# Performance work log

Measured on AMD Instinct MI355X. Metric: run time of the kernel, lower is better.

Reference implementation:

```python
import jax, jax.numpy as jnp
import numpy as np
import math

B, S, DIM = 2, 2048, 2048
NH = 16
HD = DIM // NH  # 128
RANK = 32


def setup_inputs() -> dict:
    key = jax.random.key(0)
    ks = jax.random.split(key, 10)
    x = jax.random.normal(ks[0], (B, S, DIM), dtype=jnp.float32)
    # causal additive mask (use -1e9 instead of -inf for grad-safety)
    mask = jnp.where(jnp.tril(jnp.ones((S, S), dtype=bool)), 0.0, -1e9).astype(jnp.float32)[None, None]
    # rotary frequencies, as in llama: theta = 10000^{-2i/d}
    inv_freq = 1.0 / (10000.0 ** (jnp.arange(0, HD, 2, dtype=jnp.float32) / HD))  # [HD/2]
    t = jnp.arange(S, dtype=jnp.float32)
    freqs = jnp.outer(t, inv_freq)  # [S, HD/2]
    freqs_cos = jnp.cos(freqs)
    freqs_sin = jnp.sin(freqs)
    scale = 0.02
    wq = jax.random.normal(ks[1], (DIM, DIM), dtype=jnp.float32) * scale
    wk = jax.random.normal(ks[2], (DIM, DIM), dtype=jnp.float32) * scale
    wv = jax.random.normal(ks[3], (DIM, DIM), dtype=jnp.float32) * scale
    wo = jax.random.normal(ks[4], (DIM, DIM), dtype=jnp.float32) * scale
    wa_q = jax.random.normal(ks[5], (RANK, DIM), dtype=jnp.float32) * 0.02
    wa_k = jax.random.normal(ks[6], (RANK, DIM), dtype=jnp.float32) * 0.02
    return {"x": x, "mask": mask, "freqs_cos": freqs_cos, "freqs_sin": freqs_sin,
            "wq": wq, "wk": wk, "wv": wv, "wo": wo, "wa_q": wa_q, "wa_k": wa_k}


def _apply_rope(t, cos, sin):
    # t: [B, S, H, HD]; cos/sin: [S, HD/2]
    tr = t.reshape(*t.shape[:-1], HD // 2, 2)
    tre, tim = tr[..., 0], tr[..., 1]
    c = cos[None, :, None, :]
    s = sin[None, :, None, :]
    out_re = tre * c - tim * s
    out_im = tre * s + tim * c
    return jnp.stack([out_re, out_im], axis=-1).reshape(t.shape)


def reference(x, mask, freqs_cos, freqs_sin, wq, wk, wv, wo, wa_q, wa_k):
    bsz, seqlen, dim = x.shape
    xq = (x @ wq.T).reshape(bsz, seqlen, NH, HD)
    xk = (x @ wk.T).reshape(bsz, seqlen, NH, HD)
    xv = (x @ wv.T).reshape(bsz, seqlen, NH, HD)
    # low-rank adaptive gate (computed on detached x in the original)
    xd = jax.lax.stop_gradient(x)
    xq_h = xd @ wa_q.T  # [B, S, 32]
    xk_h = xd @ wa_k.T  # [B, S, 32]
    adaptive_mask = jnp.einsum('bqr,bkr->bqk', xq_h, xk_h)  # [B, S, S]

    xq = _apply_rope(xq, freqs_cos, freqs_sin)
    xk = _apply_rope(xk, freqs_cos, freqs_sin)

    q = xq.transpose(0, 2, 1, 3)  # [B, H, S, HD]
    k = xk.transpose(0, 2, 1, 3)
    v = xv.transpose(0, 2, 1, 3)

    scores = jnp.einsum('bhqd,bhkd->bhqk', q, k) / math.sqrt(HD)
    scores = scores + mask
    scores = jax.nn.softmax(scores.astype(jnp.float32), axis=-1).astype(q.dtype)
    scores = scores * jax.nn.sigmoid(adaptive_mask)[:, None]  # gate, broadcast over heads
    out = jnp.einsum('bhqk,bhkd->bhqd', scores, v)
    out = out.transpose(0, 2, 1, 3).reshape(bsz, seqlen, -1)
    return out @ wo.T
```

## Files before the change

### kernel.cpp

```cpp
#include <hip/hip_runtime.h>

typedef __attribute__((ext_vector_type(8))) short short8v;
typedef __attribute__((ext_vector_type(4))) short short4v;
typedef __attribute__((ext_vector_type(4))) float floatx4;

#define S_    2048
#define DIM_  2048
#define NW_   6400
#define VOFF_ 4352

#define ASG(p) ((__attribute__((address_space(1))) void*)(p))
#define ASL(p) ((__attribute__((address_space(3))) void*)(p))

__device__ __forceinline__ short f2bf(float f){
  union { float f; unsigned u; } c; c.f = f;
  unsigned u = c.u;
  unsigned r = (u + 0x7fffu + ((u >> 16) & 1u)) >> 16;
  return (short)r;
}
__device__ __forceinline__ float bf2f(short s){
  union { unsigned u; float f; } c; c.u = ((unsigned)(unsigned short)s) << 16;
  return c.f;
}

__global__ __launch_bounds__(256) void cvt_k(const float* __restrict__ in,
                                             short* __restrict__ out, int n){
  int i = blockIdx.x*256 + threadIdx.x;
  int idx = i*4;
  if (idx >= n) return;
  floatx4 v = *(const floatx4*)(in + idx);
  short4v o;
  o[0]=f2bf(v[0]); o[1]=f2bf(v[1]); o[2]=f2bf(v[2]); o[3]=f2bf(v[3]);
  *(short4v*)(out + idx) = o;
}

__global__ __launch_bounds__(256)
void cvt_w(const float* wq, const float* waq, const float* wak,
           const float* wk, const float* wv, const float* wo,
           short* Wcat, short* wob){
  const float* src; short* dst; int n;
  switch (blockIdx.y){
    case 0: src=wq;  dst=Wcat;                 n=4194304; break;
    case 1: src=waq; dst=Wcat+(size_t)2048*2048; n=65536; break;
    case 2: src=wak; dst=Wcat+(size_t)2080*2048; n=65536; break;
    case 3: src=wk;  dst=Wcat+(size_t)2112*2048; n=4194304; break;
    case 4: src=wv;  dst=Wcat+(size_t)4352*2048; n=4194304; break;
    case 5: src=wo;  dst=wob;                  n=4194304; break;
    default: {
      int idx = (blockIdx.x*256 + threadIdx.x)*4;
      if (idx < 393216){
        short4v z = {0,0,0,0};
        *(short4v*)(Wcat + (size_t)4160*2048 + idx) = z;
      }
      return;
    }
  }
  int idx = (blockIdx.x*256 + threadIdx.x)*4;
  if (idx >= n) return;
  floatx4 v = *(const floatx4*)(src + idx);
  short4v o;
  o[0]=f2bf(v[0]); o[1]=f2bf(v[1]); o[2]=f2bf(v[2]); o[3]=f2bf(v[3]);
  *(short4v*)(dst + idx) = o;
}

__global__ __launch_bounds__(512,2)
void gemm_qkv(const short* __restrict__ A, const short* __restrict__ B,
              short* __restrict__ Cout, short* __restrict__ Vt){
  __shared__ short SH[65536];
  const int K = 2048;
  int tid = threadIdx.x;
  int wave = tid>>6, lane = tid&63, quad = lane>>4, l16 = lane&15;
  int wm_i = wave>>2, wn_i = wave&3;

  int bid = blockIdx.x;
  int swz = (bid&7)*50 + (bid>>3);
  int m0 = (swz & 15)*256;
  int n0 = (swz >> 4)*256;

  int srow = tid>>2;
  int sseg = (tid&3) ^ ((srow ^ (srow>>2)) & 3);
  const short* aS = A + (size_t)(m0 + srow)*K + sseg*8;
  const short* bS = B + (size_t)(n0 + srow)*K + sseg*8;
  int sdst = wave*512;

  int sx   = (l16 ^ (l16>>2)) & 3;
  int aoff = (wm_i*128 + l16)*32 + (quad^sx)*8;
  int boff = (wn_i*64  + l16)*32 + (quad^sx)*8;

  floatx4 acc[8][4] = {};

#define QSTAGE(src, chunk) do{ \
    __builtin_amdgcn_global_load_lds(ASG(src), ASL(&SH[(chunk)+sdst]), 16, 0, 0); \
    __builtin_amdgcn_global_load_lds(ASG((src) + (size_t)128*2048), ASL(&SH[(chunk)+sdst+4096]), 16, 0, 0); \
  }while(0)
#define QBAR  asm volatile("s_barrier" ::: "memory")
#define QW4   asm volatile("s_waitcnt vmcnt(4)" ::: "memory")

  QSTAGE(aS,            0);
  QSTAGE(bS,        32768);
  QSTAGE(aS+32,      8192);
  QSTAGE(bS+32, 32768+8192);
  QW4; QBAR;

  for (int t=0; t<32; ++t){
    int buf = t&1, nb = buf^1;
    int k0n = ((t+1)&31)*64;
    int A0 = buf*16384,        A1 = A0+8192;
    int B0 = 32768+buf*16384,  B1 = B0+8192;
    int nA0 = nb*16384,        nA1 = nA0+8192;
    int nB0 = 32768+nb*16384,  nB1 = nB0+8192;
    short8v af[8], bf[2];

    #pragma unroll
    for (int mf=0; mf<8; ++mf) af[mf] = *(short8v*)&SH[A0 + mf*512 + aoff];
    bf[0] = *(short8v*)&SH[B0 +   0 + boff];
    bf[1] = *(short8v*)&SH[B0 + 512 + boff];
    QSTAGE(aS + k0n, nA0);
    QBAR;
    __builtin_amdgcn_s_setprio(1);
    #pragma unroll
    for (int mf=0; mf<8; ++mf){
      acc[mf][0] = __builtin_amdgcn_mfma_f32_16x16x32_bf16(af[mf], bf[0], acc[mf][0], 0,0,0);
      acc[mf][1] = __builtin_amdgcn_mfma_f32_16x16x32_bf16(af[mf], bf[1], acc[mf][1], 0,0,0);
    }
    __builtin_amdgcn_s_setprio(0);
    QBAR;

    bf[0] = *(short8v*)&SH[B0 + 1024 + boff];
    bf[1] = *(short8v*)&SH[B0 + 1536 + boff];
    QSTAGE(bS + k0n, nB0);
    QBAR;
    __builtin_amdgcn_s_setprio(1);
    #pragma unroll
    for (int mf=0; mf<8; ++mf){
      acc[mf][2] = __builtin_amdgcn_mfma_f32_16x16x32_bf16(af[mf], bf[0], acc[mf][2], 0,0,0);
      acc[mf][3] = __builtin_amdgcn_mfma_f32_16x16x32_bf16(af[mf], bf[1], acc[mf][3], 0,0,0);
    }
    __builtin_amdgcn_s_setprio(0);
    QW4;
    QBAR;

    #pragma unroll
    for (int mf=0; mf<8; ++mf) af[mf] = *(short8v*)&SH[A1 + mf*512 + aoff];
    bf[0] = *(short8v*)&SH[B1 +   0 + boff];
    bf[1] = *(short8v*)&SH[B1 + 512 + boff];
    QSTAGE(aS + k0n + 32, nA1);
    QBAR;
    __builtin_amdgcn_s_setprio(1);
    #pragma unroll
    for (int mf=0; mf<8; ++mf){
      acc[mf][0] = __builtin_amdgcn_mfma_f32_16x16x32_bf16(af[mf], bf[0], acc[mf][0], 0,0,0);
      acc[mf][1] = __builtin_amdgcn_mfma_f32_16x16x32_bf16(af[mf], bf[1], acc[mf][1], 0,0,0);
    }
    __builtin_amdgcn_s_setprio(0);
    QBAR;

    bf[0] = *(short8v*)&SH[B1 + 1024 + boff];
    bf[1] = *(short8v*)&SH[B1 + 1536 + boff];
    QSTAGE(bS + k0n + 32, nB1);
    QBAR;
    __builtin_amdgcn_s_setprio(1);
    #pragma unroll
    for (int mf=0; mf<8; ++mf){
      acc[mf][2] = __builtin_amdgcn_mfma_f32_16x16x32_bf16(af[mf], bf[0], acc[mf][2], 0,0,0);
      acc[mf][3] = __builtin_amdgcn_mfma_f32_16x16x32_bf16(af[mf], bf[1], acc[mf][3], 0,0,0);
    }
    __builtin_amdgcn_s_setprio(0);
    QW4;
    QBAR;
  }

  __syncthreads();

  if (n0 < VOFF_){
    #pragma unroll
    for (int mf=0; mf<8; ++mf)
      #pragma unroll
      for (int r=0; r<4; ++r){
        size_t gm = (size_t)(m0 + wm_i*128 + mf*16 + quad*4 + r);
        #pragma unroll
        for (int nf=0; nf<4; ++nf)
          Cout[gm*NW_ + n0 + wn_i*64 + nf*16 + l16] = f2bf(acc[mf][nf][r]);
      }
  } else {
    short* T = SH;
    #pragma unroll
    for (int mf=0; mf<8; ++mf){
      int mb = wm_i*128 + mf*16 + quad*4;
      int mc = mb>>3, mi = mb&7;
      #pragma unroll
      for (int nf=0; nf<4; ++nf){
        int n = wn_i*64 + nf*16 + l16;
        short4v p;
        p[0]=f2bf(acc[mf][nf][0]); p[1]=f2bf(acc[mf][nf][1]);
        p[2]=f2bf(acc[mf][nf][2]); p[3]=f2bf(acc[mf][nf][3]);
        *(short4v*)&T[n*256 + ((mc ^ (n&31))*8) + mi] = p;
      }
    }
    __syncthreads();
    int f = tid>>1, half = tid&1;
    size_t vbase = (size_t)(n0 - VOFF_ + f)*4096 + m0;
    #pragma unroll
    for (int c=0; c<16; ++c){
      int cc = half*16 + c;
      short8v v = *(short8v*)&T[f*256 + ((cc ^ (f&31))*8)];
      *(short8v*)&Vt[vbase + cc*8] = v;
    }
  }
#undef QSTAGE
#undef QBAR
#undef QW4
}

__global__ __launch_bounds__(256,4)
void gemm_nt_f32(const short* __restrict__ A, const short* __restrict__ B,
                 float* __restrict__ Cout, int M, int N, int K){
  __shared__ short As[128][64];
  __shared__ short Bs[128][64];
  int tid = threadIdx.x;
  int wave = tid>>6, lane = tid&63, quad = lane>>4, l16 = lane&15;
  int l7 = l16&7;
  int m0 = blockIdx.x*128, n0 = blockIdx.y*128;
  int wm = (wave>>1)*64, wn = (wave&1)*64;
  floatx4 acc[4][4] = {};

  int lr = lane>>3;
  int sw = (lane&7) ^ lr;
  const short* Abase = A + (size_t)(m0 + wave*32 + lr)*K + sw*8;
  const short* Bbase = B + (size_t)(n0 + wave*32 + lr)*K + sw*8;

  for (int k0 = 0; k0 < K; k0 += 64){
    __syncthreads();
    #pragma unroll
    for (int i=0;i<4;i++){
      __builtin_amdgcn_global_load_lds(ASG(Abase + (size_t)(i*8)*K + k0),
                                       ASL(&As[wave*32 + i*8][0]), 16, 0, 0);
      __builtin_amdgcn_global_load_lds(ASG(Bbase + (size_t)(i*8)*K + k0),
                                       ASL(&Bs[wave*32 + i*8][0]), 16, 0, 0);
    }
    __syncthreads();
    #pragma unroll
    for (int ks=0; ks<2; ks++){
      short8v af[4], bf[4];
      #pragma unroll
      for (int i=0;i<4;i++) af[i] = *(short8v*)&As[wm + i*16 + l16][((ks*4+quad)^l7)*8];
      #pragma unroll
      for (int j=0;j<4;j++) bf[j] = *(short8v*)&Bs[wn + j*16 + l16][((ks*4+quad)^l7)*8];
      #pragma unroll
      for (int i=0;i<4;i++)
        #pragma unroll
        for (int j=0;j<4;j++)
          acc[i][j] = __builtin_amdgcn_mfma_f32_16x16x32_bf16(af[i], bf[j], acc[i][j], 0,0,0);
    }
  }
  #pragma unroll
  for (int i=0;i<4;i++)
    #pragma unroll
    for (int r=0;r<4;r++){
      int gm = m0 + wm + i*16 + quad*4 + r;
      #pragma unroll
      for (int j=0;j<4;j++){
        int gn = n0 + wn + j*16 + l16;
        Cout[(size_t)gm*N + gn] = acc[i][j][r];
      }
    }
}

__global__ __launch_bounds__(256) void rope_k(short* __restrict__ X,
                                              const float* __restrict__ fcos,
                                              const float* __restrict__ fsin){
  int i = blockIdx.x*256 + threadIdx.x;
  int row = i >> 10;
  int p = i & 1023;
  int s = row & (S_-1);
  int pp = p & 63;
  float c = fcos[s*64+pp], sn = fsin[s*64+pp];
  size_t a = (size_t)row*NW_ + 2112 + p*2;
  int v = *(int*)(X + a);
  float re = bf2f((short)(v & 0xffff)), im = bf2f((short)(v >> 16));
  float orr = re*c - im*sn, oi = re*sn + im*c;
  *(int*)(X + a) = ((int)(unsigned short)f2bf(oi) << 16) | (unsigned short)f2bf(orr);
}

__global__ __launch_bounds__(256)
void gate_k(const short* __restrict__ X, short* __restrict__ G){
  int kt = blockIdx.x, qt = blockIdx.y, b = blockIdx.z;
  if (kt > qt) return;
  int tid = threadIdx.x, wave = tid>>6, lane = tid&63, quad = lane>>4, l16 = lane&15;
  const float NL2E = -1.44269504f;

  short8v qh = *(const short8v*)&X[(size_t)(b*2048 + qt*64 + wave*16 + l16)*NW_ + 2048 + quad*8];
  floatx4 am[4];
  #pragma unroll
  for (int j=0;j<4;j++){
    short8v kh = *(const short8v*)&X[(size_t)(b*2048 + kt*64 + j*16 + l16)*NW_ + 2080 + quad*8];
    floatx4 z = {0.f,0.f,0.f,0.f};
    am[j] = __builtin_amdgcn_mfma_f32_16x16x32_bf16(qh, kh, z, 0,0,0);
  }
  short* Gd = G + (((size_t)(b*32 + kt)*2048) + qt*64 + wave*16 + quad*4)*64 + l16*4;
  #pragma unroll
  for (int r=0;r<4;r++){
    short4v sv;
    #pragma unroll
    for (int j=0;j<4;j++){
      float g = __builtin_amdgcn_rcpf(1.f + __builtin_amdgcn_exp2f(am[j][r]*NL2E));
      sv[j] = f2bf(g);
    }
    *(short4v*)(Gd + (size_t)r*64) = sv;
  }
}

__global__ __launch_bounds__(256,2)
void flash_k(const short* __restrict__ Qc, const short* __restrict__ Vt,
             const short* __restrict__ G, const float* __restrict__ fcos,
             const float* __restrict__ fsin, short* __restrict__ O){
  int h = blockIdx.x, pi = blockIdx.y, b = blockIdx.z;
  int tid = threadIdx.x, wave = tid>>6, lane = tid&63, quad = lane>>4, l16 = lane&15;
  int l7 = l16&7;

  __shared__ short Ks [64][128];
  __shared__ short Vts[128][64];
  __shared__ short Ps [4][16][72];

  const float CS = 1.44269504f * 0.08838834764831845f;

  for (int ph = 0; ph < 2; ph++){
    int qt = ph ? pi : 31 - pi;
    int srow = qt*64 + wave*16 + l16;
    size_t qrow = (size_t)(b*2048 + srow);
    short8v qf[4];
    #pragma unroll
    for (int ks=0;ks<4;ks++)
      qf[ks] = *(const short8v*)&Qc[qrow*NW_ + h*128 + ks*32 + quad*8];
    #pragma unroll
    for (int ks=0;ks<4;ks++)
      #pragma unroll
      for (int jj=0;jj<4;jj++){
        float re = bf2f(qf[ks][2*jj]), im = bf2f(qf[ks][2*jj+1]);
        int p = ks*16 + quad*4 + jj;
        float c = fcos[srow*64 + p], sn = fsin[srow*64 + p];
        qf[ks][2*jj]   = f2bf(re*c - im*sn);
        qf[ks][2*jj+1] = f2bf(re*sn + im*c);
      }

    floatx4 oacc[8] = {};
    float lp[4] = {0.f,0.f,0.f,0.f};

    for (int kt=0; kt<=qt; kt++){
      int k0 = kt*64;
      __syncthreads();
      {
        const short* Ksrc = Qc + ((size_t)(b*2048 + k0 + wave*16))*NW_ + 2112 + h*128;
        int r4 = lane>>4, c16 = lane&15;
        #pragma unroll
        for (int j=0;j<4;j++)
          __builtin_amdgcn_global_load_lds(
            ASG(Ksrc + (size_t)(j*4 + r4)*NW_ + ((c16 ^ r4 ^ ((j&1)*4))*8)),
            ASL(&Ks[wave*16 + j*4][0]), 16, 0, 0);
        const short* Vsrc = Vt + ((size_t)(h*128 + wave*32 + (lane>>3)))*4096 + b*2048 + k0
                            + (((lane&7) ^ (lane>>3))*8);
        #pragma unroll
        for (int j=0;j<4;j++)
          __builtin_amdgcn_global_load_lds(
            ASG(Vsrc + (size_t)(j*8)*4096),
            ASL(&Vts[wave*32 + j*8][0]), 16, 0, 0);
      }
      __syncthreads();

      const short* gb = G + (((size_t)(b*32 + kt)*2048) + qt*64 + wave*16 + quad*4)*64 + l16*4;
      short4v g4[4];
      #pragma unroll
      for (int r=0;r<4;r++) g4[r] = *(const short4v*)(gb + (size_t)r*64);

      floatx4 sacc[4] = {};
      #pragma unroll
      for (int j=0;j<4;j++)
        #pragma unroll
        for (int ks2=0;ks2<4;ks2++){
          short8v kf = *(short8v*)&Ks[j*16+l16][((ks2*4+quad)^l7)*8];
          sacc[j] = __builtin_amdgcn_mfma_f32_16x16x32_bf16(qf[ks2], kf, sacc[j], 0,0,0);
        }

      bool diag = (kt == qt);
      int qbase = wave*16 + quad*4;
      #pragma unroll
      for (int j=0;j<4;j++){
        int kin = j*16 + l16;
        #pragma unroll
        for (int r=0;r<4;r++){
          bool keep = !diag || (kin <= qbase + r);
          float p = keep ? __builtin_amdgcn_exp2f(sacc[j][r]*CS) : 0.f;
          lp[r] += p;
          Ps[wave][quad*4+r][j*16+l16] = f2bf(p * bf2f(g4[r][j]));
        }
      }

      #pragma unroll
      for (int ks2=0; ks2<2; ks2++){
        short8v pf = *(short8v*)&Ps[wave][l16][ks2*32 + quad*8];
        #pragma unroll
        for (int dt=0; dt<8; dt++){
          short8v vf = *(short8v*)&Vts[dt*16 + l16][((ks2*4+quad)^l7)*8];
          oacc[dt] = __builtin_amdgcn_mfma_f32_16x16x32_bf16(pf, vf, oacc[dt], 0,0,0);
        }
      }
    }

    #pragma unroll
    for (int r=0;r<4;r++)
      #pragma unroll
      for (int off=1; off<16; off<<=1)
        lp[r] += __shfl_xor(lp[r], off, 64);
    #pragma unroll
    for (int r=0;r<4;r++){
      float inv = __builtin_amdgcn_rcpf(lp[r]);
      size_t orow = (size_t)(b*2048 + qt*64 + wave*16 + quad*4 + r);
      #pragma unroll
      for (int dt=0;dt<8;dt++)
        O[orow*2048 + h*128 + dt*16 + l16] = f2bf(oacc[dt][r]*inv);
    }
  }
}

extern "C" void kernel_launch(void* const* d_in, const int* in_sizes, int n_in,
                              void* d_out, int out_size, void* d_ws, size_t ws_size,
                              hipStream_t stream){
  const float* x    = (const float*)d_in[0];
  const float* fcos = (const float*)d_in[2];
  const float* fsin = (const float*)d_in[3];
  const float* wq   = (const float*)d_in[4];
  const float* wk   = (const float*)d_in[5];
  const float* wv   = (const float*)d_in[6];
  const float* wo   = (const float*)d_in[7];
  const float* waq  = (const float*)d_in[8];
  const float* wak  = (const float*)d_in[9];
  float* out = (float*)d_out;

  char* ws = (char*)d_ws;
  size_t off = 0;
  short* xb   = (short*)(ws + off); off += (size_t)4096*2048*2;
  short* Wcat = (short*)(ws + off); off += (size_t)NW_*2048*2;
  short* wob  = (short*)(ws + off); off += (size_t)2048*2048*2;
  short* XQKV = (short*)(ws + off); off += (size_t)4096*NW_*2;
  short* Vtb  = (short*)(ws + off); off += (size_t)2048*4096*2;
  short* G    = xb;
  short* Ob   = Wcat;

  cvt_k<<<8192,256,0,stream>>>(x, xb, 8388608);
  cvt_w<<<dim3(4096,7),256,0,stream>>>(wq, waq, wak, wk, wv, wo, Wcat, wob);

  gemm_qkv<<<dim3(400),512,0,stream>>>(xb, Wcat, XQKV, Vtb);

  rope_k<<<16384,256,0,stream>>>(XQKV, fcos, fsin);
  gate_k<<<dim3(32,32,2),256,0,stream>>>(XQKV, G);

  flash_k<<<dim3(16,16,2),256,0,stream>>>(XQKV, Vtb, G, fcos, fsin, Ob);

  gemm_nt_f32<<<dim3(32,16),256,0,stream>>>(Ob, wob, out, 4096, 2048, 2048);
}
```

Measured before the change: 426.7 us.

## Restructure QKV GEMM main loop into register double-buffered ping-pong schedule

Rewrites the fused QKV projection GEMM main loop to keep two register sets of A/B fragments (afA/bfA, afB/bfB). Fragments for the next sub-step are loaded from LDS while the current MFMA quadrant runs, and each phase now issues a 4x4 MFMA block instead of 8x2. Global-to-LDS staging is reordered so loads are issued one sub-tile further ahead (kn2), with fewer barriers per iteration. The aim is to hide LDS read latency and barrier stalls behind MFMA work, at the cost of more vector registers and a more fragile ordering of buffer reuse.

```diff
diff --git a/kernel.cpp b/kernel.cpp
--- a/kernel.cpp
+++ b/kernel.cpp
@@ -88,6 +88,7 @@
   int boff = (wn_i*64  + l16)*32 + (quad^sx)*8;
 
   floatx4 acc[8][4] = {};
+  short8v afA[8], afB[8], bfA[4], bfB[4];
 
 #define QSTAGE(src, chunk) do{ \
     __builtin_amdgcn_global_load_lds(ASG(src), ASL(&SH[(chunk)+sdst]), 16, 0, 0); \
@@ -95,79 +96,82 @@
   }while(0)
 #define QBAR  asm volatile("s_barrier" ::: "memory")
 #define QW4   asm volatile("s_waitcnt vmcnt(4)" ::: "memory")
+#define MFMA_ __builtin_amdgcn_mfma_f32_16x16x32_bf16
 
   QSTAGE(aS,            0);
   QSTAGE(bS,        32768);
   QSTAGE(aS+32,      8192);
   QSTAGE(bS+32, 32768+8192);
-  QW4; QBAR;
+  QW4;
+  QBAR;
+  #pragma unroll
+  for (int mf=0; mf<4; ++mf) afA[mf] = *(short8v*)&SH[0     + mf*512 + aoff];
+  #pragma unroll
+  for (int nf=0; nf<4; ++nf) bfA[nf] = *(short8v*)&SH[32768 + nf*512 + boff];
+  QSTAGE(aS + 64, 16384);
 
   for (int t=0; t<32; ++t){
     int buf = t&1, nb = buf^1;
-    int k0n = ((t+1)&31)*64;
-    int A0 = buf*16384,        A1 = A0+8192;
-    int B0 = 32768+buf*16384,  B1 = B0+8192;
-    int nA0 = nb*16384,        nA1 = nA0+8192;
-    int nB0 = 32768+nb*16384,  nB1 = nB0+8192;
-    short8v af[8], bf[2];
-
-    #pragma unroll
-    for (int mf=0; mf<8; ++mf) af[mf] = *(short8v*)&SH[A0 + mf*512 + aoff];
-    bf[0] = *(short8v*)&SH[B0 +   0 + boff];
-    bf[1] = *(short8v*)&SH[B0 + 512 + boff];
-    QSTAGE(aS + k0n, nA0);
+    int A0c = buf*16384,        A1c = A0c+8192;
+    int B0c = 32768+buf*16384,  B1c = B0c+8192;
+    int A0n = nb*16384,         A1n = A0n+8192;
+    int B0n = 32768+nb*16384,   B1n = B0n+8192;
+    int kn  = ((t+1)&31)*64;
+    int kn2 = ((t+2)&31)*64;
+
+    #pragma unroll
+    for (int mf=4; mf<8; ++mf) afA[mf] = *(short8v*)&SH[A0c + mf*512 + aoff];
+    QSTAGE(bS + kn, B0n);
+    QW4;
     QBAR;
     __builtin_amdgcn_s_setprio(1);
     #pragma unroll
-    for (int mf=0; mf<8; ++mf){
-      acc[mf][0] = __builtin_amdgcn_mfma_f32_16x16x32_bf16(af[mf], bf[0], acc[mf][0], 0,0,0);
-      acc[mf][1] = __builtin_amdgcn_mfma_f32_16x16x32_bf16(af[mf], bf[1], acc[mf][1], 0,0,0);
-    }
+    for (int mf=0; mf<4; ++mf)
+      #pragma unroll
+      for (int nf=0; nf<4; ++nf)
+        acc[mf][nf] = MFMA_(afA[mf], bfA[nf], acc[mf][nf], 0,0,0);
     __builtin_amdgcn_s_setprio(0);
-    QBAR;
-
-    bf[0] = *(short8v*)&SH[B0 + 1024 + boff];
-    bf[1] = *(short8v*)&SH[B0 + 1536 + boff];
-    QSTAGE(bS + k0n, nB0);
+
+    #pragma unroll
+    for (int mf=0; mf<4; ++mf) afB[mf] = *(short8v*)&SH[A1c + mf*512 + aoff];
+    #pragma unroll
+    for (int nf=0; nf<4; ++nf) bfB[nf] = *(short8v*)&SH[B1c + nf*512 + boff];
+    QSTAGE(aS + kn + 32, A1n);
     QBAR;
     __builtin_amdgcn_s_setprio(1);
     #pragma unroll
-    for (int mf=0; mf<8; ++mf){
-      acc[mf][2] = __builtin_amdgcn_mfma_f32_16x16x32_bf16(af[mf], bf[0], acc[mf][2], 0,0,0);
-      acc[mf][3] = __builtin_amdgcn_mfma_f32_16x16x32_bf16(af[mf], bf[1], acc[mf][3], 0,0,0);
-    }
+    for (int mf=4; mf<8; ++mf)
+      #pragma unroll
+      for (int nf=0; nf<4; ++nf)
+        acc[mf][nf] = MFMA_(afA[mf], bfA[nf], acc[mf][nf], 0,0,0);
     __builtin_amdgcn_s_setprio(0);
+
+    #pragma unroll
+    for (int mf=4; mf<8; ++mf) afB[mf] = *(short8v*)&SH[A1c + mf*512 + aoff];
+    QSTAGE(bS + kn + 32, B1n);
     QW4;
     QBAR;
-
-    #pragma unroll
-    for (int mf=0; mf<8; ++mf) af[mf] = *(short8v*)&SH[A1 + mf*512 + aoff];
-    bf[0] = *(short8v*)&SH[B1 +   0 + boff];
-    bf[1] = *(short8v*)&SH[B1 + 512 + boff];
-    QSTAGE(aS + k0n + 32, nA1);
+    __builtin_amdgcn_s_setprio(1);
+    #pragma unroll
+    for (int mf=0; mf<4; ++mf)
+      #pragma unroll
+      for (int nf=0; nf<4; ++nf)
+        acc[mf][nf] = MFMA_(afB[mf], bfB[nf], acc[mf][nf], 0,0,0);
+    __builtin_amdgcn_s_setprio(0);
+
+    #pragma unroll
+    for (int mf=0; mf<4; ++mf) afA[mf] = *(short8v*)&SH[A0n + mf*512 + aoff];
+    #pragma unroll
+    for (int nf=0; nf<4; ++nf) bfA[nf] = *(short8v*)&SH[B0n + nf*512 + boff];
+    QSTAGE(aS + kn2, A0c);
     QBAR;
     __builtin_amdgcn_s_setprio(1);
     #pragma unroll
-    for (int mf=0; mf<8; ++mf){
-      acc[mf][0] = __builtin_amdgcn_mfma_f32_16x16x32_bf16(af[mf], bf[0], acc[mf][0], 0,0,0);
-      acc[mf][1] = __builtin_amdgcn_mfma_f32_16x16x32_bf16(af[mf], bf[1], acc[mf][1], 0,0,0);
-    }
+    for (int mf=4; mf<8; ++mf)
+      #pragma unroll
+      for (int nf=0; nf<4; ++nf)
+        acc[mf][nf] = MFMA_(afB[mf], bfB[nf], acc[mf][nf], 0,0,0);
     __builtin_amdgcn_s_setprio(0);
-    QBAR;
-
-    bf[0] = *(short8v*)&SH[B1 + 1024 + boff];
-    bf[1] = *(short8v*)&SH[B1 + 1536 + boff];
-    QSTAGE(bS + k0n + 32, nB1);
-    QBAR;
-    __builtin_amdgcn_s_setprio(1);
-    #pragma unroll
-    for (int mf=0; mf<8; ++mf){
-      acc[mf][2] = __builtin_amdgcn_mfma_f32_16x16x32_bf16(af[mf], bf[0], acc[mf][2], 0,0,0);
-      acc[mf][3] = __builtin_amdgcn_mfma_f32_16x16x32_bf16(af[mf], bf[1], acc[mf][3], 0,0,0);
-    }
-    __builtin_amdgcn_s_setprio(0);
-    QW4;
-    QBAR;
   }
 
   __syncthreads();
@@ -210,6 +214,7 @@
 #undef QSTAGE
 #undef QBAR
 #undef QW4
+#undef MFMA_
 }
 
 __global__ __launch_bounds__(256,4)
```

Result: faster. 399.8 us (-6.3%).

## Deepen QKV GEMM pipeline to four LDS stages with register double-buffering

Applied to the files above, without the earlier changes.

Restructures the main projection GEMM loop from a two-buffer scheme with four barriers per half-tile to a four-slot ring of LDS k-slices. Global-to-LDS loads are issued four slices ahead and waited on with vmcnt(8). The next slice's fragments are read into a second register set while MFMAs run on the current set. The aim is to cut barrier count and hide LDS and global latency behind MFMA work. In exchange it raises register pressure (two full fragment sets) and relies on the single barrier per slice being enough to keep the ring safe.

```diff
diff --git a/kernel.cpp b/kernel.cpp
--- a/kernel.cpp
+++ b/kernel.cpp
@@ -88,86 +88,82 @@
   int boff = (wn_i*64  + l16)*32 + (quad^sx)*8;
 
   floatx4 acc[8][4] = {};
+  short8v afA[8], bfA[4], afB[8], bfB[4];
 
 #define QSTAGE(src, chunk) do{ \
     __builtin_amdgcn_global_load_lds(ASG(src), ASL(&SH[(chunk)+sdst]), 16, 0, 0); \
     __builtin_amdgcn_global_load_lds(ASG((src) + (size_t)128*2048), ASL(&SH[(chunk)+sdst+4096]), 16, 0, 0); \
   }while(0)
 #define QBAR  asm volatile("s_barrier" ::: "memory")
-#define QW4   asm volatile("s_waitcnt vmcnt(4)" ::: "memory")
-
-  QSTAGE(aS,            0);
-  QSTAGE(bS,        32768);
-  QSTAGE(aS+32,      8192);
-  QSTAGE(bS+32, 32768+8192);
-  QW4; QBAR;
-
-  for (int t=0; t<32; ++t){
-    int buf = t&1, nb = buf^1;
-    int k0n = ((t+1)&31)*64;
-    int A0 = buf*16384,        A1 = A0+8192;
-    int B0 = 32768+buf*16384,  B1 = B0+8192;
-    int nA0 = nb*16384,        nA1 = nA0+8192;
-    int nB0 = 32768+nb*16384,  nB1 = nB0+8192;
-    short8v af[8], bf[2];
-
-    #pragma unroll
-    for (int mf=0; mf<8; ++mf) af[mf] = *(short8v*)&SH[A0 + mf*512 + aoff];
-    bf[0] = *(short8v*)&SH[B0 +   0 + boff];
-    bf[1] = *(short8v*)&SH[B0 + 512 + boff];
-    QSTAGE(aS + k0n, nA0);
-    QBAR;
+#define QW8   asm volatile("s_waitcnt vmcnt(8)" ::: "memory")
+#define MFMA_ __builtin_amdgcn_mfma_f32_16x16x32_bf16
+
+  QSTAGE(aS      ,     0);  QSTAGE(bS      , 32768      );
+  QSTAGE(aS +  32,  8192);  QSTAGE(bS +  32, 32768+ 8192);
+  QSTAGE(aS +  64, 16384);  QSTAGE(bS +  64, 32768+16384);
+  QSTAGE(aS +  96, 24576);  QSTAGE(bS +  96, 32768+24576);
+  QW8; QBAR;
+  #pragma unroll
+  for (int mf=0; mf<8; ++mf) afA[mf] = *(short8v*)&SH[        mf*512 + aoff];
+  #pragma unroll
+  for (int nf=0; nf<4; ++nf) bfA[nf] = *(short8v*)&SH[32768 + nf*512 + boff];
+
+  for (int kk=0; kk<32; ++kk){
+    int k0  = kk*2, k1 = k0+1;
+    int nr0 = ((k0+1)&3)*8192;
+    int nr1 = ((k1+1)&3)*8192;
+    int sr0 = (k0&3)*8192;
+    int sr1 = (k1&3)*8192;
+    int sk0 = ((k0+4)&63)*32;
+    int sk1 = ((k1+4)&63)*32;
+
+    #pragma unroll
+    for (int mf=0; mf<6; ++mf) afB[mf] = *(short8v*)&SH[nr0 + mf*512 + aoff];
     __builtin_amdgcn_s_setprio(1);
     #pragma unroll
     for (int mf=0; mf<8; ++mf){
-      acc[mf][0] = __builtin_amdgcn_mfma_f32_16x16x32_bf16(af[mf], bf[0], acc[mf][0], 0,0,0);
-      acc[mf][1] = __builtin_amdgcn_mfma_f32_16x16x32_bf16(af[mf], bf[1], acc[mf][1], 0,0,0);
+      acc[mf][0] = MFMA_(afA[mf], bfA[0], acc[mf][0], 0,0,0);
+      acc[mf][1] = MFMA_(afA[mf], bfA[1], acc[mf][1], 0,0,0);
     }
     __builtin_amdgcn_s_setprio(0);
-    QBAR;
-
-    bf[0] = *(short8v*)&SH[B0 + 1024 + boff];
-    bf[1] = *(short8v*)&SH[B0 + 1536 + boff];
-    QSTAGE(bS + k0n, nB0);
-    QBAR;
+    QSTAGE(aS + sk0, sr0);
+    QSTAGE(bS + sk0, 32768 + sr0);
+    afB[6] = *(short8v*)&SH[nr0 + 6*512 + aoff];
+    afB[7] = *(short8v*)&SH[nr0 + 7*512 + aoff];
+    #pragma unroll
+    for (int nf=0; nf<4; ++nf) bfB[nf] = *(short8v*)&SH[32768 + nr0 + nf*512 + boff];
+    QW8; QBAR;
     __builtin_amdgcn_s_setprio(1);
     #pragma unroll
     for (int mf=0; mf<8; ++mf){
-      acc[mf][2] = __builtin_amdgcn_mfma_f32_16x16x32_bf16(af[mf], bf[0], acc[mf][2], 0,0,0);
-      acc[mf][3] = __builtin_amdgcn_mfma_f32_16x16x32_bf16(af[mf], bf[1], acc[mf][3], 0,0,0);
+      acc[mf][2] = MFMA_(afA[mf], bfA[2], acc[mf][2], 0,0,0);
+      acc[mf][3] = MFMA_(afA[mf], bfA[3], acc[mf][3], 0,0,0);
     }
     __builtin_amdgcn_s_setprio(0);
-    QW4;
-    QBAR;
-
-    #pragma unroll
-    for (int mf=0; mf<8; ++mf) af[mf] = *(short8v*)&SH[A1 + mf*512 + aoff];
-    bf[0] = *(short8v*)&SH[B1 +   0 + boff];
-    bf[1] = *(short8v*)&SH[B1 + 512 + boff];
-    QSTAGE(aS + k0n + 32, nA1);
-    QBAR;
+
+    #pragma unroll
+    for (int mf=0; mf<6; ++mf) afA[mf] = *(short8v*)&SH[nr1 + mf*512 + aoff];
     __builtin_amdgcn_s_setprio(1);
     #pragma unroll
     for (int mf=0; mf<8; ++mf){
-      acc[mf][0] = __builtin_amdgcn_mfma_f32_16x16x32_bf16(af[mf], bf[0], acc[mf][0], 0,0,0);
-      acc[mf][1] = __builtin_amdgcn_mfma_f32_16x16x32_bf16(af[mf], bf[1], acc[mf][1], 0,0,0);
+      acc[mf][0] = MFMA_(afB[mf], bfB[0], acc[mf][0], 0,0,0);
+      acc[mf][1] = MFMA_(afB[mf], bfB[1], acc[mf][1], 0,0,0);
     }
     __builtin_amdgcn_s_setprio(0);
-    QBAR;
-
-    bf[0] = *(short8v*)&SH[B1 + 1024 + boff];
-    bf[1] = *(short8v*)&SH[B1 + 1536 + boff];
-    QSTAGE(bS + k0n + 32, nB1);
-    QBAR;
+    QSTAGE(aS + sk1, sr1);
+    QSTAGE(bS + sk1, 32768 + sr1);
+    afA[6] = *(short8v*)&SH[nr1 + 6*512 + aoff];
+    afA[7] = *(short8v*)&SH[nr1 + 7*512 + aoff];
+    #pragma unroll
+    for (int nf=0; nf<4; ++nf) bfA[nf] = *(short8v*)&SH[32768 + nr1 + nf*512 + boff];
+    QW8; QBAR;
     __builtin_amdgcn_s_setprio(1);
     #pragma unroll
     for (int mf=0; mf<8; ++mf){
-      acc[mf][2] = __builtin_amdgcn_mfma_f32_16x16x32_bf16(af[mf], bf[0], acc[mf][2], 0,0,0);
-      acc[mf][3] = __builtin_amdgcn_mfma_f32_16x16x32_bf16(af[mf], bf[1], acc[mf][3], 0,0,0);
+      acc[mf][2] = MFMA_(afB[mf], bfB[2], acc[mf][2], 0,0,0);
+      acc[mf][3] = MFMA_(afB[mf], bfB[3], acc[mf][3], 0,0,0);
     }
     __builtin_amdgcn_s_setprio(0);
-    QW4;
-    QBAR;
   }
 
   __syncthreads();
@@ -209,7 +205,8 @@
   }
 #undef QSTAGE
 #undef QBAR
-#undef QW4
+#undef QW8
+#undef MFMA_
 }
 
 __global__ __launch_bounds__(256,4)
```

Measured after the change: 402.6 us. 1.06x faster.
